# Performance work log

Hardware: AMD Instinct MI355X
Metric: run time of the kernel (lower is better)

## Reference

```python
import jax, jax.numpy as jnp
import numpy as np

B, N_DET, N_T, NY, NX = 8, 128, 2048, 256, 256


def setup_inputs() -> dict:
    key = jax.random.key(0)
    k1, k2, k3 = jax.random.split(key, 3)
    sino = jax.random.normal(k1, (B, 1, N_DET, N_T), dtype=jnp.float32)
    # LUT channel 0: fractional time index (some out-of-range to exercise valid mask)
    lut0 = jax.random.uniform(k2, (NY, NX, N_DET), dtype=jnp.float32,
                              minval=-8.0, maxval=float(N_T) + 8.0)
    alpha = jax.random.uniform(k3, (NY, NX, N_DET), dtype=jnp.float32)
    k_floor = jnp.floor(lut0)
    valid = (k_floor >= 0) & (k_floor < N_T - 1)
    k0 = jnp.clip(k_floor, 0, N_T - 2).astype(jnp.int32)
    # Hann apodization window over detectors
    win = 0.5 - 0.5 * np.cos(2.0 * np.pi * np.arange(N_DET) / max(N_DET - 1, 1))
    apod = jnp.asarray(win.astype(np.float32))
    return {"sino": sino, "alpha": alpha, "apod": apod, "k0": k0, "valid": valid}


def reference(sino, alpha, apod, k0, valid):
    # Per-sample normalization over (n_det, n_t)
    eps = jnp.finfo(sino.dtype).eps
    mean = jnp.mean(sino, axis=(-1, -2), keepdims=True)
    centered = sino - mean
    std = jnp.sqrt(jnp.mean(centered * centered, axis=(-1, -2), keepdims=True) + eps)
    S = (centered / std)[:, 0]                     # [B, n_det, n_t]

    P = NY * NX
    kd = jnp.transpose(k0, (2, 0, 1)).reshape(N_DET, P)      # [n_det, P]
    ad = jnp.transpose(alpha, (2, 0, 1)).reshape(N_DET, P)   # [n_det, P]
    vd = jnp.transpose(valid, (2, 0, 1)).reshape(N_DET, P).astype(S.dtype)

    idx0 = jnp.broadcast_to(kd[None], (B, N_DET, P))
    s0 = jnp.take_along_axis(S, idx0, axis=2)                # [B, n_det, P]
    s1 = jnp.take_along_axis(S, idx0 + 1, axis=2)            # [B, n_det, P]
    sk = ((1.0 - ad) * s0 + ad * s1) * vd                    # linear interp + mask

    out = jnp.einsum('d,bdp->bp', apod, sk).reshape(B, NY, NX)
    norm = jnp.maximum(jnp.sum(apod), jnp.finfo(apod.dtype).tiny)
    return (out / norm)[:, None]                             # [B, 1, ny, nx]
```

## Files before the change

### kernel.cpp

```cpp
#include <hip/hip_runtime.h>
#include <hip/hip_fp16.h>

#define NB    8
#define NDET  128
#define NT    2048
#define NPIX  65536
#define NELEM (NDET * NT)
#define NGRP  32


#define WS_S16_OFF   8192
#define WS_PT_OFF    (8192 + (size_t)NDET * NT * NB * 2)
#define WS7_REQUIRED (WS_PT_OFF + (size_t)NGRP * NPIX * NB * 2)
#define WS2_REQUIRED (WS_PT_OFF + (size_t)8 * NB * NPIX * 4)

__global__ __launch_bounds__(256) void k_stats(const float* __restrict__ sino,
                                               double* __restrict__ wsd) {
    const int bx = blockIdx.x;
    const int b = bx >> 5, i = bx & 31;
    const float4* src = (const float4*)(sino + (size_t)b * NELEM);
    const int base = i * 2048;
    double s = 0.0, ss = 0.0;
    for (int r = 0; r < 8; ++r) {
        float4 v = src[base + r * 256 + threadIdx.x];
        double d0 = v.x, d1 = v.y, d2 = v.z, d3 = v.w;
        s  += d0 + d1 + d2 + d3;
        ss += d0 * d0 + d1 * d1 + d2 * d2 + d3 * d3;
    }
    for (int off = 32; off; off >>= 1) {
        s  += __shfl_down(s, off);
        ss += __shfl_down(ss, off);
    }
    __shared__ double lds[8];
    const int wave = threadIdx.x >> 6;
    if ((threadIdx.x & 63) == 0) { lds[wave * 2] = s; lds[wave * 2 + 1] = ss; }
    __syncthreads();
    if (threadIdx.x == 0) {
        double S = 0, SS = 0;
        for (int w = 0; w < 4; ++w) { S += lds[w * 2]; SS += lds[w * 2 + 1]; }
        wsd[bx * 2] = S; wsd[bx * 2 + 1] = SS;
    }
}

__global__ __launch_bounds__(256) void k_finalize(const float* __restrict__ apod,
                                                  const unsigned char* __restrict__ validb,
                                                  const double* __restrict__ wsd,
                                                  float* __restrict__ wsf) {
    __shared__ float sap[NDET];
    __shared__ int sflag;
    const int t = threadIdx.x;
    if (t == 0) sflag = 0;
    if (t < NDET) sap[t] = apod[t];
    int local = 0;
    {
        const unsigned char* vb = validb + t * 256;
        for (int j = 1; j < 256; j += 4) local |= (vb[j] != 0);
    }
    __syncthreads();
    if (local) atomicOr(&sflag, 1);
    if (t < NB) {
        double S = 0, SS = 0;
        for (int i = 0; i < 32; ++i) {
            S  += wsd[(t * 32 + i) * 2];
            SS += wsd[(t * 32 + i) * 2 + 1];
        }
        double mean = S / (double)NELEM;
        double var  = SS / (double)NELEM - mean * mean;
        double istd = 1.0 / sqrt(var + (double)(1.1920928955078125e-07f));
        wsf[t]     = (float)mean;
        wsf[8 + t] = (float)istd;
    }
    if (t == 0) {
        double a = 0;
        for (int d = 0; d < NDET; ++d) a += (double)sap[d];
        float norm = fmaxf((float)a, 1.1754943508222875e-38f);
        wsf[17] = 1.0f / norm;
    }
    __syncthreads();
    if (t < NDET) wsf[32 + t] = sap[t] * wsf[17];
    if (t == 0) ((unsigned int*)wsf)[16] = (unsigned int)(sflag != 0);
}

__global__ __launch_bounds__(256) void k_build(const float* __restrict__ sino,
                                               const float* __restrict__ wsf,
                                               __half* __restrict__ S16) {
    const int dt = blockIdx.x * 256 + threadIdx.x;
    union { uint4 q; __half h[8]; } u;
#pragma unroll
    for (int b = 0; b < NB; ++b) {
        float x = sino[(size_t)b * NELEM + dt];
        u.h[b] = __float2half((x - wsf[b]) * wsf[8 + b]);
    }
    *(uint4*)(S16 + (size_t)dt * 8) = u.q;
}

__global__ __launch_bounds__(256) void k_pack(const int* __restrict__ k0,
                                              const float* __restrict__ alpha,
                                              const void* __restrict__ valid,
                                              const float* __restrict__ wsf,
                                              uint4* __restrict__ packT) {
    const unsigned int mode = ((const unsigned int*)wsf)[16];
    const int g  = threadIdx.x & 31;
    const int pl = threadIdx.x >> 5;
    const int pbase = blockIdx.x * 32;
#pragma unroll
    for (int r = 0; r < 4; ++r) {
        const int p = pbase + r * 8 + pl;
        const size_t e = (size_t)p * NDET + g * 4;
        int4   kq = *(const int4*)(k0 + e);
        float4 aq = *(const float4*)(alpha + e);
        unsigned int vb[4];
        if (mode) {
            unsigned int v = *(const unsigned int*)((const unsigned char*)valid + e);
            vb[0] = v & 0xffu; vb[1] = (v >> 8) & 0xffu;
            vb[2] = (v >> 16) & 0xffu; vb[3] = v >> 24;
        } else {
            uint4 v = *(const uint4*)((const unsigned int*)valid + e);
            vb[0] = v.x; vb[1] = v.y; vb[2] = v.z; vb[3] = v.w;
        }
        const int   ks[4] = {kq.x, kq.y, kq.z, kq.w};
        const float as[4] = {aq.x, aq.y, aq.z, aq.w};
        uint4 o;
        unsigned int* ow = (unsigned int*)&o;
#pragma unroll
        for (int j = 0; j < 4; ++j) {
            __half ha = __float2half_rn(as[j]);
            unsigned short hb = *(unsigned short*)&ha;
            ow[j] = ((unsigned int)ks[j] & 0x7FFu) | ((vb[j] ? 1u : 0u) << 11) |
                    ((unsigned int)hb << 16);
        }
        packT[(size_t)g * NPIX + p] = o;
    }
}

__device__ __forceinline__ float2 h2f(unsigned int w) {
    __half2 h;
    *reinterpret_cast<unsigned int*>(&h) = w;
    return __half22float2(h);
}

__global__ __launch_bounds__(1024) void k_das7(uint4* pk,
                                               const __half* __restrict__ S16,
                                               const float* __restrict__ wsf) {
    __shared__ __align__(16) __half SL[4 * NT * NB];
    const int x     = blockIdx.x & 7;
    const int sub   = (blockIdx.x >> 3) & 3;
    const int chunk = blockIdx.x >> 5;
    const int g     = x * 4 + sub;
    {
        const uint4* src = (const uint4*)(S16 + (size_t)g * 4 * NT * NB);
        uint4* dst = (uint4*)SL;
#pragma unroll
        for (int i = 0; i < 8; ++i)
            dst[i * 1024 + threadIdx.x] = src[i * 1024 + threadIdx.x];
    }
    __syncthreads();

    float apn[4];
#pragma unroll
    for (int j = 0; j < 4; ++j) apn[j] = wsf[32 + g * 4 + j];

    const int p0 = chunk * 8192 + (int)threadIdx.x;
    const size_t base = (size_t)g * NPIX + p0;

    uint4 pkb = pk[base];
    for (int it = 0; it < 8; ++it) {
        const uint4 pkc = pkb;
        if (it < 7) pkb = pk[base + (size_t)(it + 1) * 1024];

        const unsigned int pw[4] = {pkc.x, pkc.y, pkc.z, pkc.w};
        float acc[NB] = {0.f, 0.f, 0.f, 0.f, 0.f, 0.f, 0.f, 0.f};
#pragma unroll
        for (int j = 0; j < 4; ++j) {
            const unsigned int wj = pw[j];
            const int kk = (int)(wj & 0x7FFu);
            unsigned short hb = (unsigned short)(wj >> 16);
            const float aa = __half2float(*(const __half*)&hb);
            const float w  = (wj & 0x800u) ? apn[j] : 0.0f;
            const float wb = w * aa;
            const float wa = w - wb;
            const uint4* s = (const uint4*)(SL + ((size_t)(j * NT + kk) << 3));
            uint4 q0 = s[0];
            uint4 q1 = s[1];
            const unsigned int w0[4] = {q0.x, q0.y, q0.z, q0.w};
            const unsigned int w1[4] = {q1.x, q1.y, q1.z, q1.w};
#pragma unroll
            for (int h = 0; h < 4; ++h) {
                float2 f0 = h2f(w0[h]);
                float2 f1 = h2f(w1[h]);
                acc[2 * h]     += wa * f0.x + wb * f1.x;
                acc[2 * h + 1] += wa * f0.y + wb * f1.y;
            }
        }
        union { uint4 q; __half2 h[4]; } o;
#pragma unroll
        for (int h = 0; h < 4; ++h)
            o.h[h] = __floats2half2_rn(acc[2 * h], acc[2 * h + 1]);
        pk[base + (size_t)it * 1024] = o.q;
    }
}

__global__ __launch_bounds__(256) void k_reduce2(const __half* __restrict__ pT,
                                                 float* __restrict__ out) {
    const int p = blockIdx.x * 256 + threadIdx.x;
    float acc[NB] = {0.f, 0.f, 0.f, 0.f, 0.f, 0.f, 0.f, 0.f};
#pragma unroll
    for (int g = 0; g < NGRP; ++g) {
        union { uint4 q; __half2 h[4]; } u;
        u.q = *(const uint4*)(pT + ((size_t)g * NPIX + p) * NB);
#pragma unroll
        for (int h = 0; h < 4; ++h) {
            float2 f = __half22float2(u.h[h]);
            acc[2 * h]     += f.x;
            acc[2 * h + 1] += f.y;
        }
    }
#pragma unroll
    for (int b = 0; b < NB; ++b)
        out[(size_t)b * NPIX + p] = acc[b];
}

__global__ __launch_bounds__(1024) void k_das2(const int* __restrict__ k0,
                                               const float* __restrict__ alpha,
                                               const void* __restrict__ valid,
                                               const __half* __restrict__ S16,
                                               const float* __restrict__ wsf,
                                               float* __restrict__ partials) {
    const int px = threadIdx.x & 255;
    const int dc = threadIdx.x >> 8;
    const int slice = blockIdx.x & 7;
    const int chunk = blockIdx.x >> 3;
    const int p  = chunk * 256 + px;
    const int d0 = slice * 16 + dc * 4;
    const unsigned int mode = ((const unsigned int*)wsf)[16];
    const float* apodn = wsf + 32;

    float acc[NB] = {0.f, 0.f, 0.f, 0.f, 0.f, 0.f, 0.f, 0.f};
    const size_t lbase = (size_t)p * NDET + d0;

    int4   k4 = *(const int4*)(k0 + lbase);
    float4 a4 = *(const float4*)(alpha + lbase);
    unsigned int vbits;
    if (mode) {
        unsigned int v4 = *(const unsigned int*)((const unsigned char*)valid + lbase);
        vbits = ((v4 & 0xffu) ? 1u : 0u) | (((v4 >> 8) & 0xffu) ? 2u : 0u) |
                (((v4 >> 16) & 0xffu) ? 4u : 0u) | ((v4 >> 24) ? 8u : 0u);
    } else {
        uint4 v4 = *(const uint4*)((const unsigned int*)valid + lbase);
        vbits = (v4.x ? 1u : 0u) | (v4.y ? 2u : 0u) | (v4.z ? 4u : 0u) | (v4.w ? 8u : 0u);
    }
    const int   kk[4] = {k4.x, k4.y, k4.z, k4.w};
    const float aa[4] = {a4.x, a4.y, a4.z, a4.w};
#pragma unroll
    for (int j = 0; j < 4; ++j) {
        const int d = d0 + j;
        const float w  = ((vbits >> j) & 1u) ? apodn[d] : 0.0f;
        const float wb = w * aa[j];
        const float wa = w - wb;
        const uint4* s = (const uint4*)(S16 + ((size_t)(d * NT + kk[j]) << 3));
        uint4 q0 = s[0];
        uint4 q1 = s[1];
        const unsigned int w0[4] = {q0.x, q0.y, q0.z, q0.w};
        const unsigned int w1[4] = {q1.x, q1.y, q1.z, q1.w};
#pragma unroll
        for (int h = 0; h < 4; ++h) {
            float2 f0 = h2f(w0[h]);
            float2 f1 = h2f(w1[h]);
            acc[2 * h]     += wa * f0.x + wb * f1.x;
            acc[2 * h + 1] += wa * f0.y + wb * f1.y;
        }
    }

    __shared__ float red[1024][9];
#pragma unroll
    for (int b = 0; b < NB; ++b) red[threadIdx.x][b] = acc[b];
    __syncthreads();
    if (dc == 0) {
#pragma unroll
        for (int b = 0; b < NB; ++b) {
            float v = red[px][b] + red[px + 256][b] + red[px + 512][b] + red[px + 768][b];
            partials[((size_t)slice * NB + b) * NPIX + p] = v;
        }
    }
}

__global__ __launch_bounds__(256) void k_reduce(const float* __restrict__ partials,
                                                float* __restrict__ out) {
    const int i = (blockIdx.x * 256 + threadIdx.x) * 4;
    float4 s = {0.f, 0.f, 0.f, 0.f};
#pragma unroll
    for (int g = 0; g < 8; ++g) {
        float4 v = *(const float4*)(partials + (size_t)g * NB * NPIX + i);
        s.x += v.x; s.y += v.y; s.z += v.z; s.w += v.w;
    }
    *(float4*)(out + i) = s;
}

extern "C" void kernel_launch(void* const* d_in, const int* in_sizes, int n_in,
                              void* d_out, int out_size, void* d_ws, size_t ws_size,
                              hipStream_t stream) {
    const float* sino  = (const float*)d_in[0];
    const float* alpha = (const float*)d_in[1];
    const float* apod  = (const float*)d_in[2];
    const int*   k0    = (const int*)d_in[3];
    const void*  valid = d_in[4];

    float*  out = (float*)d_out;
    double* wsd = (double*)d_ws;
    float*  wsf = (float*)((char*)d_ws + 4096);
    __half* S16 = (__half*)((char*)d_ws + WS_S16_OFF);
    uint4*  pk  = (uint4*)((char*)d_ws + WS_PT_OFF);
    float*  parts = (float*)((char*)d_ws + WS_PT_OFF);

    k_stats   <<<256,  256, 0, stream>>>(sino, wsd);
    k_finalize<<<1,    256, 0, stream>>>(apod, (const unsigned char*)valid, wsd, wsf);
    k_build   <<<1024, 256, 0, stream>>>(sino, wsf, S16);
    if (ws_size >= WS7_REQUIRED) {
        k_pack   <<<2048, 256, 0, stream>>>(k0, alpha, valid, wsf, pk);
        k_das7   <<<256, 1024, 0, stream>>>(pk, S16, wsf);
        k_reduce2<<<256,  256, 0, stream>>>((const __half*)pk, out);
    } else {
        k_das2  <<<2048, 1024, 0, stream>>>(k0, alpha, valid, S16, wsf, parts);
        k_reduce<<<512,   256, 0, stream>>>(parts, out);
    }
}
```

Measured before the change: 67.74 us.

## Fuse LUT packing into DAS kernel and tile partials layout for reduce

Removes the separate k_pack kernel and its global round-trip of packed LUT data. The DAS kernel now loads k0, alpha and valid directly, with coalesced loads spread across four sibling blocks' quarters. Each block packs only its own group into a shared-memory staging buffer per 1024-pixel segment, with software prefetch of the next segment. Partial outputs are written in a pixel-tile-major layout so the reduce reads contiguous 64-pixel tiles across groups. The cost is extra __syncthreads per segment, and each block reads four times the LUT data it uses.

```diff
diff --git a/kernel.cpp b/kernel.cpp
--- a/kernel.cpp
+++ b/kernel.cpp
@@ -7,12 +7,12 @@
 #define NPIX  65536
 #define NELEM (NDET * NT)
 #define NGRP  32
+#define SEGPX 1024
 
 
 #define WS_S16_OFF   8192
 #define WS_PT_OFF    (8192 + (size_t)NDET * NT * NB * 2)
 #define WS7_REQUIRED (WS_PT_OFF + (size_t)NGRP * NPIX * NB * 2)
-#define WS2_REQUIRED (WS_PT_OFF + (size_t)8 * NB * NPIX * 4)
 
 __global__ __launch_bounds__(256) void k_stats(const float* __restrict__ sino,
                                                double* __restrict__ wsd) {
@@ -94,59 +94,25 @@
     *(uint4*)(S16 + (size_t)dt * 8) = u.q;
 }
 
-__global__ __launch_bounds__(256) void k_pack(const int* __restrict__ k0,
-                                              const float* __restrict__ alpha,
-                                              const void* __restrict__ valid,
-                                              const float* __restrict__ wsf,
-                                              uint4* __restrict__ packT) {
-    const unsigned int mode = ((const unsigned int*)wsf)[16];
-    const int g  = threadIdx.x & 31;
-    const int pl = threadIdx.x >> 5;
-    const int pbase = blockIdx.x * 32;
-#pragma unroll
-    for (int r = 0; r < 4; ++r) {
-        const int p = pbase + r * 8 + pl;
-        const size_t e = (size_t)p * NDET + g * 4;
-        int4   kq = *(const int4*)(k0 + e);
-        float4 aq = *(const float4*)(alpha + e);
-        unsigned int vb[4];
-        if (mode) {
-            unsigned int v = *(const unsigned int*)((const unsigned char*)valid + e);
-            vb[0] = v & 0xffu; vb[1] = (v >> 8) & 0xffu;
-            vb[2] = (v >> 16) & 0xffu; vb[3] = v >> 24;
-        } else {
-            uint4 v = *(const uint4*)((const unsigned int*)valid + e);
-            vb[0] = v.x; vb[1] = v.y; vb[2] = v.z; vb[3] = v.w;
-        }
-        const int   ks[4] = {kq.x, kq.y, kq.z, kq.w};
-        const float as[4] = {aq.x, aq.y, aq.z, aq.w};
-        uint4 o;
-        unsigned int* ow = (unsigned int*)&o;
-#pragma unroll
-        for (int j = 0; j < 4; ++j) {
-            __half ha = __float2half_rn(as[j]);
-            unsigned short hb = *(unsigned short*)&ha;
-            ow[j] = ((unsigned int)ks[j] & 0x7FFu) | ((vb[j] ? 1u : 0u) << 11) |
-                    ((unsigned int)hb << 16);
-        }
-        packT[(size_t)g * NPIX + p] = o;
-    }
-}
-
 __device__ __forceinline__ float2 h2f(unsigned int w) {
     __half2 h;
     *reinterpret_cast<unsigned int*>(&h) = w;
     return __half22float2(h);
 }
 
-__global__ __launch_bounds__(1024) void k_das7(uint4* pk,
+__global__ __launch_bounds__(1024) void k_das8(const int* __restrict__ k0,
+                                               const float* __restrict__ alpha,
+                                               const void* __restrict__ valid,
                                                const __half* __restrict__ S16,
-                                               const float* __restrict__ wsf) {
+                                               const float* __restrict__ wsf,
+                                               uint4* __restrict__ pT) {
     __shared__ __align__(16) __half SL[4 * NT * NB];
+    __shared__ __align__(16) uint4  PL[SEGPX];
     const int x     = blockIdx.x & 7;
     const int sub   = (blockIdx.x >> 3) & 3;
     const int chunk = blockIdx.x >> 5;
     const int g     = x * 4 + sub;
+
     {
         const uint4* src = (const uint4*)(S16 + (size_t)g * 4 * NT * NB);
         uint4* dst = (uint4*)SL;
@@ -154,20 +120,72 @@
         for (int i = 0; i < 8; ++i)
             dst[i * 1024 + threadIdx.x] = src[i * 1024 + threadIdx.x];
     }
-    __syncthreads();
-
+
+    const unsigned int mode = ((const unsigned int*)wsf)[16];
     float apn[4];
 #pragma unroll
     for (int j = 0; j < 4; ++j) apn[j] = wsf[32 + g * 4 + j];
 
-    const int p0 = chunk * 8192 + (int)threadIdx.x;
-    const size_t base = (size_t)g * NPIX + p0;
-
-    uint4 pkb = pk[base];
-    for (int it = 0; it < 8; ++it) {
-        const uint4 pkc = pkb;
-        if (it < 7) pkb = pk[base + (size_t)(it + 1) * 1024];
-
+    const int t   = (int)threadIdx.x;
+    const int q   = t & 3;
+    const int pxl = t >> 2;
+    const int p0  = chunk * 8192;
+    const bool mine = (q == sub);
+
+    int4         kq[4];
+    float4       aq[4];
+    unsigned int vq[4];
+
+#define LOADSEG(SEG)                                                          \
+    {                                                                         \
+        _Pragma("unroll")                                                     \
+        for (int r = 0; r < 4; ++r) {                                         \
+            const int p = p0 + (SEG) * SEGPX + r * 256 + pxl;                 \
+            const size_t e = (size_t)p * NDET + x * 16 + q * 4;               \
+            kq[r] = *(const int4*)(k0 + e);                                   \
+            aq[r] = *(const float4*)(alpha + e);                              \
+            if (mode) {                                                       \
+                vq[r] = *(const unsigned int*)((const unsigned char*)valid + e); \
+            } else {                                                          \
+                uint4 v = *(const uint4*)((const unsigned int*)valid + e);    \
+                vq[r] = (v.x ? 1u : 0u) | (v.y ? 2u : 0u) |                   \
+                        (v.z ? 4u : 0u) | (v.w ? 8u : 0u);                    \
+            }                                                                 \
+        }                                                                     \
+    }
+
+#define PACKSEG                                                               \
+    if (mine) {                                                               \
+        _Pragma("unroll")                                                     \
+        for (int r = 0; r < 4; ++r) {                                         \
+            unsigned int vm = mode ? (((vq[r] & 0xffu) ? 1u : 0u) |           \
+                                      ((vq[r] & 0xff00u) ? 2u : 0u) |         \
+                                      ((vq[r] & 0xff0000u) ? 4u : 0u) |       \
+                                      ((vq[r] & 0xff000000u) ? 8u : 0u))      \
+                                   : vq[r];                                   \
+            const int   ks[4] = {kq[r].x, kq[r].y, kq[r].z, kq[r].w};         \
+            const float as[4] = {aq[r].x, aq[r].y, aq[r].z, aq[r].w};         \
+            uint4 o;                                                          \
+            unsigned int* ow = (unsigned int*)&o;                             \
+            _Pragma("unroll")                                                 \
+            for (int j = 0; j < 4; ++j) {                                     \
+                __half ha = __float2half_rn(as[j]);                           \
+                unsigned short hb = *(unsigned short*)&ha;                    \
+                ow[j] = ((unsigned int)ks[j] & 0x7FFu) |                      \
+                        (((vm >> j) & 1u) << 11) | ((unsigned int)hb << 16);  \
+            }                                                                 \
+            PL[r * 256 + pxl] = o;                                            \
+        }                                                                     \
+    }
+
+    LOADSEG(0)
+    PACKSEG
+    __syncthreads();
+
+    for (int seg = 0; seg < 8; ++seg) {
+        if (seg < 7) LOADSEG(seg + 1)
+
+        const uint4 pkc = PL[t];
         const unsigned int pw[4] = {pkc.x, pkc.y, pkc.z, pkc.w};
         float acc[NB] = {0.f, 0.f, 0.f, 0.f, 0.f, 0.f, 0.f, 0.f};
 #pragma unroll
@@ -192,22 +210,33 @@
                 acc[2 * h + 1] += wa * f0.y + wb * f1.y;
             }
         }
-        union { uint4 q; __half2 h[4]; } o;
+        union { uint4 qq; __half2 h[4]; } o;
 #pragma unroll
         for (int h = 0; h < 4; ++h)
             o.h[h] = __floats2half2_rn(acc[2 * h], acc[2 * h + 1]);
-        pk[base + (size_t)it * 1024] = o.q;
-    }
+        const int p = p0 + seg * SEGPX + t;
+        pT[(size_t)(p >> 6) * 2048 + g * 64 + (p & 63)] = o.qq;
+
+        __syncthreads();
+        if (seg < 7) {
+            PACKSEG
+            __syncthreads();
+        }
+    }
+#undef LOADSEG
+#undef PACKSEG
 }
 
 __global__ __launch_bounds__(256) void k_reduce2(const __half* __restrict__ pT,
                                                  float* __restrict__ out) {
     const int p = blockIdx.x * 256 + threadIdx.x;
+    const int tile = p >> 6, pl = p & 63;
+    const uint4* pq = (const uint4*)pT;
     float acc[NB] = {0.f, 0.f, 0.f, 0.f, 0.f, 0.f, 0.f, 0.f};
 #pragma unroll
     for (int g = 0; g < NGRP; ++g) {
         union { uint4 q; __half2 h[4]; } u;
-        u.q = *(const uint4*)(pT + ((size_t)g * NPIX + p) * NB);
+        u.q = pq[(size_t)tile * 2048 + g * 64 + pl];
 #pragma unroll
         for (int h = 0; h < 4; ++h) {
             float2 f = __half22float2(u.h[h]);
@@ -309,16 +338,15 @@
     double* wsd = (double*)d_ws;
     float*  wsf = (float*)((char*)d_ws + 4096);
     __half* S16 = (__half*)((char*)d_ws + WS_S16_OFF);
-    uint4*  pk  = (uint4*)((char*)d_ws + WS_PT_OFF);
+    uint4*  pT  = (uint4*)((char*)d_ws + WS_PT_OFF);
     float*  parts = (float*)((char*)d_ws + WS_PT_OFF);
 
     k_stats   <<<256,  256, 0, stream>>>(sino, wsd);
     k_finalize<<<1,    256, 0, stream>>>(apod, (const unsigned char*)valid, wsd, wsf);
     k_build   <<<1024, 256, 0, stream>>>(sino, wsf, S16);
     if (ws_size >= WS7_REQUIRED) {
-        k_pack   <<<2048, 256, 0, stream>>>(k0, alpha, valid, wsf, pk);
-        k_das7   <<<256, 1024, 0, stream>>>(pk, S16, wsf);
-        k_reduce2<<<256,  256, 0, stream>>>((const __half*)pk, out);
+        k_das8   <<<256, 1024, 0, stream>>>(k0, alpha, valid, S16, wsf, pT);
+        k_reduce2<<<256,  256, 0, stream>>>((const __half*)pT, out);
     } else {
         k_das2  <<<2048, 1024, 0, stream>>>(k0, alpha, valid, S16, wsf, parts);
         k_reduce<<<512,   256, 0, stream>>>(parts, out);
```

Result: slower. 83.18 us (+22.8%).
